# Kernel optimization log

Measured on AMD Instinct MI355X. Metric: run time of the kernel, lower is better.

## Reference

```python
import jax, jax.numpy as jnp
import numpy as np

# Loihi neuron / simulation constants (params['neuron'], params['simulation'])
VTH_MANT = 80
V_DECAY = 128
I_DECAY = 1024
REF_DELAY = 1
WGT_EXP = 0
TAU_RHO = 1.0
SCALE_RHO = 1.0
TS = 1
THETA = float(VTH_MANT * (1 << 6))      # 5120, Loihi threshold in fixed-point units
W_SCALE = float(1 << (6 + WGT_EXP))     # 64, weight scaling into Loihi fixed point


def st_floor(x):
    """floor with straight-through gradient (Loihi integer truncation)."""
    return x + jax.lax.stop_gradient(jnp.floor(x) - x)


@jax.custom_vjp
def spike_fn(v):
    # binary spike scaled by 1/Ts, as in SLAYER-Loihi
    return (v >= THETA).astype(v.dtype) * (1.0 / TS)

def _spike_fwd(v):
    return spike_fn(v), v

def _spike_bwd(v, g):
    # SLAYER surrogate: scaleRho/(tauRho*theta) * exp(-|v - theta| / (tauRho*theta))
    pdf = (SCALE_RHO / (TAU_RHO * THETA)) * jnp.exp(-jnp.abs(v - THETA) / (TAU_RHO * THETA))
    return (g * pdf,)

spike_fn.defvjp(_spike_fwd, _spike_bwd)


def quantize_w(w, step=2.0):
    """SLAYER snn.utils.quantize(w, 2) with straight-through gradient."""
    return w + jax.lax.stop_gradient(jnp.round(w / step) * step - w)


def loihi_spikes(wsp):
    """Loihi CUBA neuron scan. wsp: [T, B, C] weighted spike input -> [T, B, C] spikes."""
    i_mul = (4096.0 - I_DECAY) / 4096.0
    v_mul = (4096.0 - V_DECAY) / 4096.0

    def step(carry, x):
        I, V, ref = carry
        I = st_floor(I * i_mul) + W_SCALE * x
        V = st_floor(V * v_mul) + I
        V = jnp.where(ref > 0, jnp.zeros_like(V), V)   # refractory hold at 0
        s = spike_fn(V)
        V = V * (1.0 - s * TS)                          # reset to 0 on spike
        ref = jnp.where(s > 0, REF_DELAY - 1, jnp.maximum(ref - 1, 0))
        return (I, V, ref), s

    B, C = wsp.shape[1], wsp.shape[2]
    init = (jnp.zeros((B, C), wsp.dtype),
            jnp.zeros((B, C), wsp.dtype),
            jnp.zeros((B, C), jnp.int32))
    _, s = jax.lax.scan(step, init, wsp)
    return s


def delay_shift(x):
    """delayShift(x, 1): shift spikes one step forward in time. x: [T, B, C]."""
    return jnp.concatenate([jnp.zeros_like(x[:1]), x[:-1]], axis=0)


def setup_inputs() -> dict:
    key = jax.random.key(0)
    k1, k2, k3 = jax.random.split(key, 3)
    B, IN, HID, OUT, T = 32, 1024, 2048, 512, 256
    spike_input = (jax.random.uniform(k1, (B, IN, T)) < 0.05).astype(jnp.float32)
    W1 = jax.random.normal(k2, (HID, IN), jnp.float32) * 8.0
    W2 = jax.random.normal(k3, (OUT, HID), jnp.float32) * 8.0
    return {"spike_input": spike_input, "W1": W1, "W2": W2}


def reference(spike_input, W1, W2):
    # spike_input: [B, IN, T] binary spikes
    x = jnp.transpose(spike_input, (2, 0, 1))          # [T, B, IN]
    w1 = quantize_w(W1)
    w2 = quantize_w(W2)
    h = jnp.einsum('tbi,hi->tbh', x, w1)               # fc1 per timestep
    s1 = delay_shift(loihi_spikes(h))                  # spikeLoihi + delayShift(1)
    o = jnp.einsum('tbh,oh->tbo', s1, w2)              # fc2 per timestep
    s2 = delay_shift(loihi_spikes(o))
    return jnp.transpose(s2, (1, 2, 0))                # [B, OUT, T]
```

## Files before the change

kernel.cpp:

```cpp
#include <hip/hip_runtime.h>

typedef unsigned char u8;
typedef signed char i8;
typedef unsigned int u32;
typedef __attribute__((ext_vector_type(4))) int i32x4;

#define AS1 __attribute__((address_space(1)))
#define AS3 __attribute__((address_space(3)))

__device__ __forceinline__ void gload_lds16(const void* g, void* l) {
    __builtin_amdgcn_global_load_lds((const AS1 void*)g, (AS3 void*)l, 16, 0, 0);
}

__global__ void transpose_x_bt(const float* __restrict__ X, i8* __restrict__ Xb,
                               int B, int IN, int T) {
    __shared__ float tile[128][33];
    const int t0 = blockIdx.x * 32, i0 = blockIdx.y * 128, b = blockIdx.z;
    const int tx = threadIdx.x & 31, ty = threadIdx.x >> 5;
    const float* src = X + (size_t)b * IN * T;
#pragma unroll
    for (int r = 0; r < 16; ++r) {
        int i = ty + r * 8;
        tile[i][tx] = src[(size_t)(i0 + i) * T + t0 + tx];
    }
    __syncthreads();
    const int cx = threadIdx.x & 31;
    const int tl0 = threadIdx.x >> 5;
#pragma unroll
    for (int r = 0; r < 4; ++r) {
        int tl = tl0 + r * 8;
        uchar4 pk;
        pk.x = (tile[cx * 4 + 0][tl] != 0.f) ? 1 : 0;
        pk.y = (tile[cx * 4 + 1][tl] != 0.f) ? 1 : 0;
        pk.z = (tile[cx * 4 + 2][tl] != 0.f) ? 1 : 0;
        pk.w = (tile[cx * 4 + 3][tl] != 0.f) ? 1 : 0;
        *(uchar4*)&Xb[((size_t)b * T + t0 + tl) * IN + i0 + cx * 4] = pk;
    }
}

__global__ void quant_both(const float4* __restrict__ W1, const float4* __restrict__ W2,
                           char4* __restrict__ W1q, char4* __restrict__ W2q,
                           int n1v, int n2v) {
    int i = blockIdx.x * 256 + threadIdx.x;
    if (i < n1v) {
        float4 w = W1[i];
        char4 q;
        q.x = (i8)(int)rintf(w.x * 0.5f);
        q.y = (i8)(int)rintf(w.y * 0.5f);
        q.z = (i8)(int)rintf(w.z * 0.5f);
        q.w = (i8)(int)rintf(w.w * 0.5f);
        W1q[i] = q;
    } else if (i < n1v + n2v) {
        int j = i - n1v;
        float4 w = W2[j];
        char4 q;
        q.x = (i8)(int)rintf(w.x * 0.5f);
        q.y = (i8)(int)rintf(w.y * 0.5f);
        q.z = (i8)(int)rintf(w.z * 0.5f);
        q.w = (i8)(int)rintf(w.w * 0.5f);
        W2q[j] = q;
    }
}

__global__ __launch_bounds__(512, 4) void gemm1_scan1(
        const i8* __restrict__ A, const i8* __restrict__ Bt,
        i8* __restrict__ S1, int K) {
    __shared__ __align__(16) i8 lds[69632];
    i8*    lA   = lds;
    i8*    lB   = lds + 32768;
    short* hT   = (short*)lds;
    u32*   bits = (u32*)(lds + 65536);

    const int nwg = gridDim.x;
    const int cpx = nwg >> 3;
    const int wg  = (blockIdx.x & 7) * cpx + (blockIdx.x >> 3);
    const int bx = wg & 15;
    const int by = wg >> 4;
    const int n0 = bx * 128;
    const int m0 = by * 256;

    const int tid  = threadIdx.x;
    const int lane = tid & 63;
    const int w    = tid >> 6;
    const int wm   = w & 3;
    const int wn   = w >> 2;
    const int l15 = lane & 15;
    const int l4  = lane >> 4;
    const int sw  = l15 & 7;

    i32x4 acc[4][4] = {};
    const int flatT = tid * 16;

    for (int k0 = 0; k0 < K; k0 += 128) {
        __syncthreads();
#pragma unroll
        for (int q = 0; q < 4; ++q) {
            int fl = q * 8192 + flatT;
            int r  = fl >> 7;
            int sc = ((fl >> 4) & 7) ^ (r & 7);
            gload_lds16(A + (size_t)(m0 + r) * K + k0 + sc * 16, &lA[fl]);
        }
#pragma unroll
        for (int q = 0; q < 2; ++q) {
            int fl = q * 8192 + flatT;
            int r  = fl >> 7;
            int sc = ((fl >> 4) & 7) ^ (r & 7);
            gload_lds16(Bt + (size_t)(n0 + r) * K + k0 + sc * 16, &lB[fl]);
        }
        __syncthreads();
#pragma unroll
        for (int kk = 0; kk < 2; ++kk) {
            i32x4 af[4], bf[4];
#pragma unroll
            for (int mf = 0; mf < 4; ++mf)
                af[mf] = *(const i32x4*)&lA[(wm * 64 + mf * 16 + l15) * 128 +
                                            ((kk * 4 + l4) ^ sw) * 16];
#pragma unroll
            for (int nf = 0; nf < 4; ++nf)
                bf[nf] = *(const i32x4*)&lB[(wn * 64 + nf * 16 + l15) * 128 +
                                            ((kk * 4 + l4) ^ sw) * 16];
#pragma unroll
            for (int mf = 0; mf < 4; ++mf)
#pragma unroll
                for (int nf = 0; nf < 4; ++nf)
                    acc[mf][nf] = __builtin_amdgcn_mfma_i32_16x16x64_i8(
                        af[mf], bf[nf], acc[mf][nf], 0, 0, 0);
        }
    }
    __syncthreads();

#pragma unroll
    for (int mf = 0; mf < 4; ++mf)
#pragma unroll
        for (int nf = 0; nf < 4; ++nf) {
            int n = wn * 64 + nf * 16 + l15;
            int c = wm * 16 + mf * 4 + l4;
            int h0 = acc[mf][nf][0] * 2, h1 = acc[mf][nf][1] * 2;
            int h2 = acc[mf][nf][2] * 2, h3 = acc[mf][nf][3] * 2;
            int2 pk;
            pk.x = (h0 & 0xffff) | (h1 << 16);
            pk.y = (h2 & 0xffff) | (h3 << 16);
            *(int2*)((char*)hT + n * 512 + ((c ^ (n & 15)) << 3)) = pk;
        }
    __syncthreads();

    {
        const int ssel = blockIdx.x & 3;
        const int w1   = 4 + ((ssel + 1) & 3);
        const int nbase = (w == ssel) ? 0 : (w == w1) ? 64 : -1;
        if (nbase >= 0) {
            const int n = nbase + lane;
            const int nx = n & 15;
            const char* hrow = (char*)hT + n * 512;
            int2 ra[4], rb[4];
#pragma unroll
            for (int q = 0; q < 4; ++q)
                ra[q] = *(const int2*)(hrow + ((q ^ nx) << 3));
            u32 bw[8] = {0, 0, 0, 0, 0, 0, 0, 0};
            float I = 0.f, V = 0.f;
#pragma unroll
            for (int p = 0; p < 16; ++p) {
                if (p < 15) {
#pragma unroll
                    for (int q = 0; q < 4; ++q) {
                        int2 v = *(const int2*)(hrow + ((((p + 1) * 4 + q) ^ nx) << 3));
                        if (p & 1) ra[q] = v; else rb[q] = v;
                    }
                }
#pragma unroll
                for (int q = 0; q < 4; ++q) {
                    int2 hh = (p & 1) ? rb[q] : ra[q];
#pragma unroll
                    for (int j = 0; j < 4; ++j) {
                        int t = p * 16 + q * 4 + j;
                        short hv = (j == 0) ? (short)hh.x
                                 : (j == 1) ? (short)(hh.x >> 16)
                                 : (j == 2) ? (short)hh.y
                                            : (short)(hh.y >> 16);
                        I = floorf(I * 0.75f) + 64.f * (float)hv;
                        V = floorf(V * 0.96875f) + I;
                        if (V >= 5120.f) { bw[t >> 5] |= (1u << (t & 31)); V = 0.f; }
                    }
                }
            }
#pragma unroll
            for (int wi = 0; wi < 8; ++wi) bits[wi * 128 + n] = bw[wi];
        }
    }
    __syncthreads();

#pragma unroll
    for (int rep = 0; rep < 16; ++rep) {
        int d   = rep * 512 + tid;
        int tt  = d >> 5;
        int ndq = d & 31;
        u32 outw = 0;
        if (tt > 0) {
            int tb = tt - 1, wi = tb >> 5, sh = tb & 31;
            outw =  ((bits[wi * 128 + ndq * 4 + 0] >> sh) & 1)
                 | (((bits[wi * 128 + ndq * 4 + 1] >> sh) & 1) << 8)
                 | (((bits[wi * 128 + ndq * 4 + 2] >> sh) & 1) << 16)
                 | (((bits[wi * 128 + ndq * 4 + 3] >> sh) & 1) << 24);
        }
        *(u32*)&S1[(size_t)(m0 + tt) * 2048 + n0 + ndq * 4] = outw;
    }
}

__global__ __launch_bounds__(1024, 1) void gemm2_scan2(
        const i8* __restrict__ A, const i8* __restrict__ Bt,
        float* __restrict__ out, int K) {
    __shared__ __align__(16) i8 lds[83968];
    float* hT   = (float*)lds;
    u32*   bits = (u32*)(lds + 81920);

    const int nwg = gridDim.x;
    const int cpx = nwg >> 3;
    const int wg  = (blockIdx.x & 7) * cpx + (blockIdx.x >> 3);
    const int scanw = (blockIdx.x >> 3) & 15;
    const int ox = wg & 7;
    const int by = wg >> 3;
    const int n0 = ox * 64;
    const int m0 = by * 256;

    const int tid  = threadIdx.x;
    const int lane = tid & 63;
    const int w    = tid >> 6;
    const int l15 = lane & 15;
    const int l4  = lane >> 4;
    const int sw  = l15 & 7;

    i32x4 acc[4] = {};
    const int flatT = tid * 16;

    auto STAGE = [&](int buf, int k0) {
        i8* lA = lds + buf * 40960;
        i8* lB = lA + 32768;
#pragma unroll
        for (int q = 0; q < 2; ++q) {
            int fl = q * 16384 + flatT;
            int r  = fl >> 7;
            int sc = ((fl >> 4) & 7) ^ (r & 7);
            gload_lds16(A + (size_t)(m0 + r) * K + k0 + sc * 16, &lA[fl]);
        }
        if (tid < 512) {
            int fl = flatT;
            int r  = fl >> 7;
            int sc = ((fl >> 4) & 7) ^ (r & 7);
            gload_lds16(Bt + (size_t)(n0 + r) * K + k0 + sc * 16, &lB[fl]);
        }
    };

    auto COMPUTE = [&](int buf) {
        const i8* lA = lds + buf * 40960;
        const i8* lB = lA + 32768;
#pragma unroll
        for (int kk = 0; kk < 2; ++kk) {
            i32x4 af, bf[4];
            af = *(const i32x4*)&lA[(w * 16 + l15) * 128 + ((kk * 4 + l4) ^ sw) * 16];
#pragma unroll
            for (int nf = 0; nf < 4; ++nf)
                bf[nf] = *(const i32x4*)&lB[(nf * 16 + l15) * 128 +
                                            ((kk * 4 + l4) ^ sw) * 16];
#pragma unroll
            for (int nf = 0; nf < 4; ++nf)
                acc[nf] = __builtin_amdgcn_mfma_i32_16x16x64_i8(
                    af, bf[nf], acc[nf], 0, 0, 0);
        }
    };

    STAGE(0, 0);
    __syncthreads();
    int cur = 0;
    for (int k0 = 0; k0 < K; k0 += 128) {
        if (k0 + 128 < K) STAGE(cur ^ 1, k0 + 128);
        COMPUTE(cur);
        __syncthreads();
        cur ^= 1;
    }

#pragma unroll
    for (int nf = 0; nf < 4; ++nf) {
        int n = nf * 16 + l15;
        int c = w * 4 + l4;
        float4 pk;
        pk.x = (float)(acc[nf][0] * 2);
        pk.y = (float)(acc[nf][1] * 2);
        pk.z = (float)(acc[nf][2] * 2);
        pk.w = (float)(acc[nf][3] * 2);
        *(float4*)((char*)hT + n * 1024 + ((c ^ (n & 15)) << 4)) = pk;
    }
    __syncthreads();

    if (w == scanw) {
        const int n = lane;
        const int nx = n & 15;
        const char* hrow = (char*)hT + n * 1024;
        float4 ra[4], rb[4];
#pragma unroll
        for (int q = 0; q < 4; ++q)
            ra[q] = *(const float4*)(hrow + ((q ^ nx) << 4));
        u32 bw[8] = {0, 0, 0, 0, 0, 0, 0, 0};
        float I = 0.f, V = 0.f;
#pragma unroll
        for (int p = 0; p < 16; ++p) {
            if (p < 15) {
#pragma unroll
                for (int q = 0; q < 4; ++q) {
                    float4 v = *(const float4*)(hrow + ((((p + 1) * 4 + q) ^ nx) << 4));
                    if (p & 1) ra[q] = v; else rb[q] = v;
                }
            }
#pragma unroll
            for (int q = 0; q < 4; ++q) {
                float4 hh = (p & 1) ? rb[q] : ra[q];
#pragma unroll
                for (int j = 0; j < 4; ++j) {
                    int t = p * 16 + q * 4 + j;
                    float hv = (j == 0) ? hh.x : (j == 1) ? hh.y
                             : (j == 2) ? hh.z : hh.w;
                    I = floorf(I * 0.75f) + 64.f * hv;
                    V = floorf(V * 0.96875f) + I;
                    if (V >= 5120.f) { bw[t >> 5] |= (1u << (t & 31)); V = 0.f; }
                }
            }
        }
#pragma unroll
        for (int wi = 0; wi < 8; ++wi) bits[wi * 64 + n] = bw[wi];
    }
    __syncthreads();

#pragma unroll
    for (int rep = 0; rep < 4; ++rep) {
        int flat = rep * 1024 + tid;
        int o  = flat >> 6;
        int t4 = flat & 63;
        float4 v;
#pragma unroll
        for (int j = 0; j < 4; ++j) {
            int tt = t4 * 4 + j;
            float s = 0.f;
            if (tt > 0) {
                int tb = tt - 1;
                s = (float)((bits[(tb >> 5) * 64 + o] >> (tb & 31)) & 1);
            }
            if (j == 0) v.x = s; else if (j == 1) v.y = s;
            else if (j == 2) v.z = s; else v.w = s;
        }
        *(float4*)&out[((size_t)by * 512 + n0 + o) * 256 + t4 * 4] = v;
    }
}

extern "C" void kernel_launch(void* const* d_in, const int* in_sizes, int n_in,
                              void* d_out, int out_size, void* d_ws, size_t ws_size,
                              hipStream_t stream) {
    const int B = 32, IN = 1024, HID = 2048, OUT = 512, T = 256;
    const float* spikes = (const float*)d_in[0];
    const float* W1 = (const float*)d_in[1];
    const float* W2 = (const float*)d_in[2];
    float* out = (float*)d_out;

    char* ws = (char*)d_ws;
    size_t off = 0;
    auto alloc = [&](size_t bytes) -> void* {
        void* p = ws + off;
        off += (bytes + 255) & ~(size_t)255;
        return p;
    };
    i8* Xb  = (i8*)alloc((size_t)B * T * IN);
    i8* W1q = (i8*)alloc((size_t)HID * IN);
    i8* W2q = (i8*)alloc((size_t)OUT * HID);
    i8* S1  = (i8*)alloc((size_t)B * T * HID);

    transpose_x_bt<<<dim3(T / 32, IN / 128, B), dim3(256), 0, stream>>>(spikes, Xb, B, IN, T);
    {
        int n1v = HID * IN / 4, n2v = OUT * HID / 4;
        quant_both<<<dim3((n1v + n2v + 255) / 256), dim3(256), 0, stream>>>(
            (const float4*)W1, (const float4*)W2, (char4*)W1q, (char4*)W2q, n1v, n2v);
    }
    gemm1_scan1<<<dim3(512), dim3(512), 0, stream>>>(Xb, W1q, S1, IN);
    gemm2_scan2<<<dim3(256), dim3(1024), 0, stream>>>(S1, W2q, out, HID);
}
```

Baseline: 64.33 us.

## Double-buffer gemm1 K-loop and use vmcnt-based waits in both GEMMs

gemm1's single-buffered 128-wide K loop becomes a double-buffered 64-wide pipeline with a new 4-chunk XOR swizzle, so global-to-LDS loads of the next tile overlap MFMA work. Both GEMMs now use explicit s_waitcnt vmcnt counts plus raw s_barrier and sched_barrier instead of __syncthreads, so a wave waits only for its own older loads, and K is hardcoded so the loops fully unroll. This relies on the per-wave outstanding load counts being exactly right. It also hardcodes problem sizes.

```diff
diff --git a/kernel.cpp b/kernel.cpp
--- a/kernel.cpp
+++ b/kernel.cpp
@@ -10,6 +10,13 @@
 
 __device__ __forceinline__ void gload_lds16(const void* g, void* l) {
     __builtin_amdgcn_global_load_lds((const AS1 void*)g, (AS3 void*)l, 16, 0, 0);
+}
+
+template <int N>
+__device__ __forceinline__ void vm_wait() {
+    if constexpr (N == 0)      asm volatile("s_waitcnt vmcnt(0)" ::: "memory");
+    else if constexpr (N == 2) asm volatile("s_waitcnt vmcnt(2)" ::: "memory");
+    else if constexpr (N == 3) asm volatile("s_waitcnt vmcnt(3)" ::: "memory");
 }
 
 __global__ void transpose_x_bt(const float* __restrict__ X, i8* __restrict__ Xb,
@@ -64,10 +71,9 @@
 
 __global__ __launch_bounds__(512, 4) void gemm1_scan1(
         const i8* __restrict__ A, const i8* __restrict__ Bt,
-        i8* __restrict__ S1, int K) {
+        i8* __restrict__ S1) {
+    const int K = 1024;
     __shared__ __align__(16) i8 lds[69632];
-    i8*    lA   = lds;
-    i8*    lB   = lds + 32768;
     short* hT   = (short*)lds;
     u32*   bits = (u32*)(lds + 65536);
 
@@ -86,46 +92,60 @@
     const int wn   = w >> 2;
     const int l15 = lane & 15;
     const int l4  = lane >> 4;
-    const int sw  = l15 & 7;
+    const int sw  = (l15 >> 1) & 3;
 
     i32x4 acc[4][4] = {};
-    const int flatT = tid * 16;
-
-    for (int k0 = 0; k0 < K; k0 += 128) {
-        __syncthreads();
-#pragma unroll
-        for (int q = 0; q < 4; ++q) {
-            int fl = q * 8192 + flatT;
-            int r  = fl >> 7;
-            int sc = ((fl >> 4) & 7) ^ (r & 7);
+
+    auto STAGE = [&](int buf, int k0) {
+        i8* lA = lds + buf * 24576;
+        i8* lB = lA + 16384;
+#pragma unroll
+        for (int q = 0; q < 2; ++q) {
+            int fl = q * 8192 + tid * 16;
+            int r  = fl >> 6;
+            int sc = ((fl >> 4) & 3) ^ ((r >> 1) & 3);
             gload_lds16(A + (size_t)(m0 + r) * K + k0 + sc * 16, &lA[fl]);
         }
-#pragma unroll
-        for (int q = 0; q < 2; ++q) {
-            int fl = q * 8192 + flatT;
-            int r  = fl >> 7;
-            int sc = ((fl >> 4) & 7) ^ (r & 7);
+        {
+            int fl = tid * 16;
+            int r  = fl >> 6;
+            int sc = ((fl >> 4) & 3) ^ ((r >> 1) & 3);
             gload_lds16(Bt + (size_t)(n0 + r) * K + k0 + sc * 16, &lB[fl]);
         }
-        __syncthreads();
-#pragma unroll
-        for (int kk = 0; kk < 2; ++kk) {
-            i32x4 af[4], bf[4];
-#pragma unroll
-            for (int mf = 0; mf < 4; ++mf)
-                af[mf] = *(const i32x4*)&lA[(wm * 64 + mf * 16 + l15) * 128 +
-                                            ((kk * 4 + l4) ^ sw) * 16];
+    };
+
+    auto COMPUTE = [&](int buf) {
+        const i8* lA = lds + buf * 24576;
+        const i8* lB = lA + 16384;
+        i32x4 af[4], bf[4];
+#pragma unroll
+        for (int mf = 0; mf < 4; ++mf)
+            af[mf] = *(const i32x4*)&lA[(wm * 64 + mf * 16 + l15) * 64 +
+                                        ((l4 ^ sw) << 4)];
+#pragma unroll
+        for (int nf = 0; nf < 4; ++nf)
+            bf[nf] = *(const i32x4*)&lB[(wn * 64 + nf * 16 + l15) * 64 +
+                                        ((l4 ^ sw) << 4)];
+#pragma unroll
+        for (int mf = 0; mf < 4; ++mf)
 #pragma unroll
             for (int nf = 0; nf < 4; ++nf)
-                bf[nf] = *(const i32x4*)&lB[(wn * 64 + nf * 16 + l15) * 128 +
-                                            ((kk * 4 + l4) ^ sw) * 16];
-#pragma unroll
-            for (int mf = 0; mf < 4; ++mf)
-#pragma unroll
-                for (int nf = 0; nf < 4; ++nf)
-                    acc[mf][nf] = __builtin_amdgcn_mfma_i32_16x16x64_i8(
-                        af[mf], bf[nf], acc[mf][nf], 0, 0, 0);
-        }
+                acc[mf][nf] = __builtin_amdgcn_mfma_i32_16x16x64_i8(
+                    af[mf], bf[nf], acc[mf][nf], 0, 0, 0);
+    };
+
+    STAGE(0, 0);
+    STAGE(1, 64);
+#pragma unroll
+    for (int t = 0; t < 16; ++t) {
+        const int cur = t & 1;
+        if (t < 15) vm_wait<3>(); else vm_wait<0>();
+        __builtin_amdgcn_s_barrier();
+        __builtin_amdgcn_sched_barrier(0);
+        COMPUTE(cur);
+        __builtin_amdgcn_sched_barrier(0);
+        __builtin_amdgcn_s_barrier();
+        if (t < 14) STAGE(cur, (t + 2) * 64);
     }
     __syncthreads();
 
@@ -208,7 +228,8 @@
 
 __global__ __launch_bounds__(1024, 1) void gemm2_scan2(
         const i8* __restrict__ A, const i8* __restrict__ Bt,
-        float* __restrict__ out, int K) {
+        float* __restrict__ out) {
+    const int K = 2048;
     __shared__ __align__(16) i8 lds[83968];
     float* hT   = (float*)lds;
     u32*   bits = (u32*)(lds + 81920);
@@ -269,14 +290,23 @@
     };
 
     STAGE(0, 0);
-    __syncthreads();
-    int cur = 0;
-    for (int k0 = 0; k0 < K; k0 += 128) {
-        if (k0 + 128 < K) STAGE(cur ^ 1, k0 + 128);
+    STAGE(1, 128);
+#pragma unroll
+    for (int t = 0; t < 16; ++t) {
+        const int cur = t & 1;
+        if (t < 15) {
+            if (w < 8) vm_wait<3>(); else vm_wait<2>();
+        } else {
+            vm_wait<0>();
+        }
+        __builtin_amdgcn_s_barrier();
+        __builtin_amdgcn_sched_barrier(0);
         COMPUTE(cur);
-        __syncthreads();
-        cur ^= 1;
-    }
+        __builtin_amdgcn_sched_barrier(0);
+        __builtin_amdgcn_s_barrier();
+        if (t < 14) STAGE(cur, (t + 2) * 128);
+    }
+    __syncthreads();
 
 #pragma unroll
     for (int nf = 0; nf < 4; ++nf) {
@@ -377,6 +407,6 @@
         quant_both<<<dim3((n1v + n2v + 255) / 256), dim3(256), 0, stream>>>(
             (const float4*)W1, (const float4*)W2, (char4*)W1q, (char4*)W2q, n1v, n2v);
     }
-    gemm1_scan1<<<dim3(512), dim3(512), 0, stream>>>(Xb, W1q, S1, IN);
-    gemm2_scan2<<<dim3(256), dim3(1024), 0, stream>>>(S1, W2q, out, HID);
-}
+    gemm1_scan1<<<dim3(512), dim3(512), 0, stream>>>(Xb, W1q, S1);
+    gemm2_scan2<<<dim3(256), dim3(1024), 0, stream>>>(S1, W2q, out);
+}
```

Measured after the change: 64.73 us. No clear change (+0.6%).

## Fuse prep kernels and retile gemm2 to 32-column tiles with 512 threads

Applied to the files above, without the earlier changes.

Merges the input transpose/binarize and weight quantization into one launch, removing one kernel launch. Retiles gemm2_scan2 from 64 output columns per 1024-thread block to 32 columns per 512-thread block. This doubles the grid to 512 blocks and lowers LDS use so up to 4 blocks can share a CU. Each wave now covers 64 rows by 16 columns, loading four A fragments against one B fragment. Only half a wave runs the serial scan, and A-tile traffic per output column doubles.

```diff
diff --git a/kernel.cpp b/kernel.cpp
--- a/kernel.cpp
+++ b/kernel.cpp
@@ -12,10 +12,39 @@
     __builtin_amdgcn_global_load_lds((const AS1 void*)g, (AS3 void*)l, 16, 0, 0);
 }
 
-__global__ void transpose_x_bt(const float* __restrict__ X, i8* __restrict__ Xb,
-                               int B, int IN, int T) {
+__global__ void prep(const float* __restrict__ X, i8* __restrict__ Xb,
+                     const float4* __restrict__ W1, const float4* __restrict__ W2,
+                     char4* __restrict__ W1q, char4* __restrict__ W2q) {
+    const int n1v = 2048 * 1024 / 4, n2v = 512 * 2048 / 4;
     __shared__ float tile[128][33];
-    const int t0 = blockIdx.x * 32, i0 = blockIdx.y * 128, b = blockIdx.z;
+    int bid = blockIdx.x;
+    if (bid < 3072) {
+        int i = bid * 256 + threadIdx.x;
+        if (i < n1v) {
+            float4 w = W1[i];
+            char4 q;
+            q.x = (i8)(int)rintf(w.x * 0.5f);
+            q.y = (i8)(int)rintf(w.y * 0.5f);
+            q.z = (i8)(int)rintf(w.z * 0.5f);
+            q.w = (i8)(int)rintf(w.w * 0.5f);
+            W1q[i] = q;
+        } else {
+            int j = i - n1v;
+            if (j < n2v) {
+                float4 w = W2[j];
+                char4 q;
+                q.x = (i8)(int)rintf(w.x * 0.5f);
+                q.y = (i8)(int)rintf(w.y * 0.5f);
+                q.z = (i8)(int)rintf(w.z * 0.5f);
+                q.w = (i8)(int)rintf(w.w * 0.5f);
+                W2q[j] = q;
+            }
+        }
+        return;
+    }
+    bid -= 3072;
+    const int B = 32, IN = 1024, T = 256;
+    const int t0 = (bid & 7) * 32, i0 = ((bid >> 3) & 7) * 128, b = bid >> 6;
     const int tx = threadIdx.x & 31, ty = threadIdx.x >> 5;
     const float* src = X + (size_t)b * IN * T;
 #pragma unroll
@@ -35,30 +64,6 @@
         pk.z = (tile[cx * 4 + 2][tl] != 0.f) ? 1 : 0;
         pk.w = (tile[cx * 4 + 3][tl] != 0.f) ? 1 : 0;
         *(uchar4*)&Xb[((size_t)b * T + t0 + tl) * IN + i0 + cx * 4] = pk;
-    }
-}
-
-__global__ void quant_both(const float4* __restrict__ W1, const float4* __restrict__ W2,
-                           char4* __restrict__ W1q, char4* __restrict__ W2q,
-                           int n1v, int n2v) {
-    int i = blockIdx.x * 256 + threadIdx.x;
-    if (i < n1v) {
-        float4 w = W1[i];
-        char4 q;
-        q.x = (i8)(int)rintf(w.x * 0.5f);
-        q.y = (i8)(int)rintf(w.y * 0.5f);
-        q.z = (i8)(int)rintf(w.z * 0.5f);
-        q.w = (i8)(int)rintf(w.w * 0.5f);
-        W1q[i] = q;
-    } else if (i < n1v + n2v) {
-        int j = i - n1v;
-        float4 w = W2[j];
-        char4 q;
-        q.x = (i8)(int)rintf(w.x * 0.5f);
-        q.y = (i8)(int)rintf(w.y * 0.5f);
-        q.z = (i8)(int)rintf(w.z * 0.5f);
-        q.w = (i8)(int)rintf(w.w * 0.5f);
-        W2q[j] = q;
     }
 }
 
@@ -206,44 +211,46 @@
     }
 }
 
-__global__ __launch_bounds__(1024, 1) void gemm2_scan2(
+__global__ __launch_bounds__(512, 4) void gemm2_scan2(
         const i8* __restrict__ A, const i8* __restrict__ Bt,
-        float* __restrict__ out, int K) {
-    __shared__ __align__(16) i8 lds[83968];
+        float* __restrict__ out) {
+    const int K = 2048;
+    __shared__ __align__(16) i8 lds[74752];
     float* hT   = (float*)lds;
-    u32*   bits = (u32*)(lds + 81920);
+    u32*   bits = (u32*)(lds + 73728);
 
     const int nwg = gridDim.x;
     const int cpx = nwg >> 3;
     const int wg  = (blockIdx.x & 7) * cpx + (blockIdx.x >> 3);
-    const int scanw = (blockIdx.x >> 3) & 15;
-    const int ox = wg & 7;
-    const int by = wg >> 3;
-    const int n0 = ox * 64;
+    const int scanw = (blockIdx.x >> 6) & 7;
+    const int ox = wg & 15;
+    const int by = wg >> 4;
+    const int n0 = ox * 32;
     const int m0 = by * 256;
 
     const int tid  = threadIdx.x;
     const int lane = tid & 63;
     const int w    = tid >> 6;
+    const int wmq  = w & 3;
+    const int wn   = w >> 2;
     const int l15 = lane & 15;
     const int l4  = lane >> 4;
     const int sw  = l15 & 7;
 
     i32x4 acc[4] = {};
-    const int flatT = tid * 16;
 
     auto STAGE = [&](int buf, int k0) {
-        i8* lA = lds + buf * 40960;
+        i8* lA = lds + buf * 36864;
         i8* lB = lA + 32768;
 #pragma unroll
-        for (int q = 0; q < 2; ++q) {
-            int fl = q * 16384 + flatT;
+        for (int q = 0; q < 4; ++q) {
+            int fl = q * 8192 + tid * 16;
             int r  = fl >> 7;
             int sc = ((fl >> 4) & 7) ^ (r & 7);
             gload_lds16(A + (size_t)(m0 + r) * K + k0 + sc * 16, &lA[fl]);
         }
-        if (tid < 512) {
-            int fl = flatT;
+        if (tid < 256) {
+            int fl = tid * 16;
             int r  = fl >> 7;
             int sc = ((fl >> 4) & 7) ^ (r & 7);
             gload_lds16(Bt + (size_t)(n0 + r) * K + k0 + sc * 16, &lB[fl]);
@@ -251,20 +258,20 @@
     };
 
     auto COMPUTE = [&](int buf) {
-        const i8* lA = lds + buf * 40960;
+        const i8* lA = lds + buf * 36864;
         const i8* lB = lA + 32768;
 #pragma unroll
         for (int kk = 0; kk < 2; ++kk) {
-            i32x4 af, bf[4];
-            af = *(const i32x4*)&lA[(w * 16 + l15) * 128 + ((kk * 4 + l4) ^ sw) * 16];
-#pragma unroll
-            for (int nf = 0; nf < 4; ++nf)
-                bf[nf] = *(const i32x4*)&lB[(nf * 16 + l15) * 128 +
+            i32x4 af[4], bf;
+#pragma unroll
+            for (int mf = 0; mf < 4; ++mf)
+                af[mf] = *(const i32x4*)&lA[(wmq * 64 + mf * 16 + l15) * 128 +
                                             ((kk * 4 + l4) ^ sw) * 16];
-#pragma unroll
-            for (int nf = 0; nf < 4; ++nf)
-                acc[nf] = __builtin_amdgcn_mfma_i32_16x16x64_i8(
-                    af, bf[nf], acc[nf], 0, 0, 0);
+            bf = *(const i32x4*)&lB[(wn * 16 + l15) * 128 + ((kk * 4 + l4) ^ sw) * 16];
+#pragma unroll
+            for (int mf = 0; mf < 4; ++mf)
+                acc[mf] = __builtin_amdgcn_mfma_i32_16x16x64_i8(
+                    af[mf], bf, acc[mf], 0, 0, 0);
         }
     };
 
@@ -279,19 +286,19 @@
     }
 
 #pragma unroll
-    for (int nf = 0; nf < 4; ++nf) {
-        int n = nf * 16 + l15;
-        int c = w * 4 + l4;
+    for (int mf = 0; mf < 4; ++mf) {
+        int n = wn * 16 + l15;
+        int c = wmq * 16 + mf * 4 + l4;
         float4 pk;
-        pk.x = (float)(acc[nf][0] * 2);
-        pk.y = (float)(acc[nf][1] * 2);
-        pk.z = (float)(acc[nf][2] * 2);
-        pk.w = (float)(acc[nf][3] * 2);
+        pk.x = (float)(acc[mf][0] * 2);
+        pk.y = (float)(acc[mf][1] * 2);
+        pk.z = (float)(acc[mf][2] * 2);
+        pk.w = (float)(acc[mf][3] * 2);
         *(float4*)((char*)hT + n * 1024 + ((c ^ (n & 15)) << 4)) = pk;
     }
     __syncthreads();
 
-    if (w == scanw) {
+    if (w == scanw && lane < 32) {
         const int n = lane;
         const int nx = n & 15;
         const char* hrow = (char*)hT + n * 1024;
@@ -325,13 +332,13 @@
             }
         }
 #pragma unroll
-        for (int wi = 0; wi < 8; ++wi) bits[wi * 64 + n] = bw[wi];
+        for (int wi = 0; wi < 8; ++wi) bits[wi * 32 + n] = bw[wi];
     }
     __syncthreads();
 
 #pragma unroll
     for (int rep = 0; rep < 4; ++rep) {
-        int flat = rep * 1024 + tid;
+        int flat = rep * 512 + tid;
         int o  = flat >> 6;
         int t4 = flat & 63;
         float4 v;
@@ -341,7 +348,7 @@
             float s = 0.f;
             if (tt > 0) {
                 int tb = tt - 1;
-                s = (float)((bits[(tb >> 5) * 64 + o] >> (tb & 31)) & 1);
+                s = (float)((bits[(tb >> 5) * 32 + o] >> (tb & 31)) & 1);
             }
             if (j == 0) v.x = s; else if (j == 1) v.y = s;
             else if (j == 2) v.z = s; else v.w = s;
@@ -371,12 +378,9 @@
     i8* W2q = (i8*)alloc((size_t)OUT * HID);
     i8* S1  = (i8*)alloc((size_t)B * T * HID);
 
-    transpose_x_bt<<<dim3(T / 32, IN / 128, B), dim3(256), 0, stream>>>(spikes, Xb, B, IN, T);
-    {
-        int n1v = HID * IN / 4, n2v = OUT * HID / 4;
-        quant_both<<<dim3((n1v + n2v + 255) / 256), dim3(256), 0, stream>>>(
-            (const float4*)W1, (const float4*)W2, (char4*)W1q, (char4*)W2q, n1v, n2v);
-    }
+    prep<<<dim3(5120), dim3(256), 0, stream>>>(
+        spikes, Xb, (const float4*)W1, (const float4*)W2,
+        (char4*)W1q, (char4*)W2q);
     gemm1_scan1<<<dim3(512), dim3(512), 0, stream>>>(Xb, W1q, S1, IN);
-    gemm2_scan2<<<dim3(256), dim3(1024), 0, stream>>>(S1, W2q, out, HID);
-}
+    gemm2_scan2<<<dim3(512), dim3(512), 0, stream>>>(S1, W2q, out);
+}
```

Measured after the change: 62.19 us. 1.03x faster.
